# Kernel tuning notes

Hardware: AMD Instinct MI355X
Metric: run time of the kernel (lower is better)

## Reference

```python
import jax, jax.numpy as jnp
import numpy as np

B, N, C, H = 4, 1024, 768, 12
D = C // H
SCALE = D ** -0.5


def setup_inputs() -> dict:
    key = jax.random.key(0)
    k1, k2, k3, k4 = jax.random.split(key, 4)
    x1 = jax.random.normal(k1, (B, N, C), dtype=jnp.float32)
    x2 = jax.random.normal(k2, (B, N, C), dtype=jnp.float32)
    # shared (dual-stream) Linear2 weights, torch nn.Linear layout: [out, in]
    W_qkv = jax.random.normal(k3, (3 * C, C), dtype=jnp.float32) * (C ** -0.5)
    b_qkv = jnp.zeros((3 * C,), dtype=jnp.float32)
    W_proj = jax.random.normal(k4, (C, C), dtype=jnp.float32) * (C ** -0.5)
    b_proj = jnp.zeros((C,), dtype=jnp.float32)
    return {"x1": x1, "x2": x2, "W_qkv": W_qkv, "b_qkv": b_qkv,
            "W_proj": W_proj, "b_proj": b_proj}


def _split_qkv(x, W_qkv, b_qkv):
    qkv = (x @ W_qkv.T + b_qkv).reshape(B, N, 3, H, D)
    qkv = jnp.transpose(qkv, (2, 0, 3, 1, 4))  # [3,B,H,N,D]
    return qkv[0], qkv[1], qkv[2]


def reference(x1, x2, W_qkv, b_qkv, W_proj, b_proj):
    q1, k1, v1 = _split_qkv(x1, W_qkv, b_qkv)
    q2, k2, v2 = _split_qkv(x2, W_qkv, b_qkv)
    # two score maps, combined before a single shared softmax
    s1 = jnp.einsum("bhqd,bhkd->bhqk", q1 * SCALE, k1)
    s2 = jnp.einsum("bhqd,bhkd->bhqk", q2 * SCALE, k2)
    attn = jax.nn.softmax(s1 + s2, axis=-1)  # [B,H,N,N]
    # same attention matrix applied to both value streams
    o1 = jnp.einsum("bhqk,bhkd->bhqd", attn, v1)
    o2 = jnpum = jnp.einsum("bhqk,bhkd->bhqd", attn, v2) if False else jnp.einsum("bhqk,bhkd->bhqd", attn, v2)
    o1 = jnp.transpose(o1, (0, 2, 1, 3)).reshape(B, N, C)
    o2 = jnp.transpose(o2, (0, 2, 1, 3)).reshape(B, N, C)
    y1 = o1 @ W_proj.T + b_proj
    y2 = o2 @ W_proj.T + b_proj
    return y1, y2
```

## Files before the change

kernel.cpp:

```cpp
#include <hip/hip_runtime.h>
#include <hip/hip_bf16.h>


typedef __bf16 bf16x8 __attribute__((ext_vector_type(8)));
typedef __bf16 bf16x4 __attribute__((ext_vector_type(4)));
typedef float  f32x4  __attribute__((ext_vector_type(4)));

__device__ __forceinline__ bf16x8 cvt8(const float* p) {
    f32x4 f0 = *(const f32x4*)p;
    f32x4 f1 = *(const f32x4*)(p + 4);
    bf16x8 r;
    r[0] = (__bf16)f0[0]; r[1] = (__bf16)f0[1]; r[2] = (__bf16)f0[2]; r[3] = (__bf16)f0[3];
    r[4] = (__bf16)f1[0]; r[5] = (__bf16)f1[1]; r[6] = (__bf16)f1[2]; r[7] = (__bf16)f1[3];
    return r;
}

__device__ __forceinline__ void async16(const __bf16* g, __bf16* l) {
    __builtin_amdgcn_global_load_lds(
        (const __attribute__((address_space(1))) void*)g,
        (__attribute__((address_space(3))) void*)l, 16, 0, 0);
}

__global__ __launch_bounds__(256)
void cvt4_k(const float* __restrict__ x1, const float* __restrict__ x2,
            const float* __restrict__ wq, const float* __restrict__ wp,
            __bf16* __restrict__ xc, __bf16* __restrict__ wqc,
            __bf16* __restrict__ wpc)
{
    __shared__ __bf16 L[16][776];
    const int bid = blockIdx.x, t = threadIdx.x;
    const float* src; __bf16* dst; int G;
    if (bid < 256)      { src = x1; dst = xc;            G = bid; }
    else if (bid < 512) { src = x2; dst = xc + 3145728;  G = bid - 256; }
    else if (bid < 656) { src = wq; dst = wqc;           G = bid - 512; }
    else                { src = wp; dst = wpc;           G = bid - 656; }

    const float* sb = src + (size_t)G * 16 * 768;
#pragma unroll
    for (int k = 0; k < 6; k++) {
        int iv = k * 256 + t;
        int row = iv / 96, c8 = iv % 96;
        *(bf16x8*)&L[row][c8 * 8] = cvt8(sb + row * 768 + c8 * 8);
    }
    __syncthreads();
    __bf16* db = dst + (size_t)G * 12288;
#pragma unroll
    for (int k = 0; k < 6; k++) {
        int j = k * 256 + t;
        int r = j & 15, ks = (j >> 4) & 3, kt = j >> 6;
        *(bf16x8*)(db + (size_t)j * 8) = *(const bf16x8*)&L[r][kt * 32 + ks * 8];
    }
}

__global__ __launch_bounds__(256)
void cvt_kt(const float* __restrict__ src, __bf16* __restrict__ dst, int nrun) {
    int j = blockIdx.x * 256 + threadIdx.x;
    if (j >= nrun) return;
    const int r  = j & 15;
    const int ks = (j >> 4) & 3;
    const int t2 = j >> 6;
    const int kt = t2 % 24;
    const int G  = t2 / 24;
    *(bf16x8*)(dst + (size_t)j * 8) =
        cvt8(src + (size_t)(G * 16 + r) * 768 + kt * 32 + ks * 8);
}

__global__ __launch_bounds__(256)
void gemm_qkv_s(const __bf16* __restrict__ Xc, const __bf16* __restrict__ Wq,
                const float* __restrict__ bias,
                __bf16* __restrict__ qo, __bf16* __restrict__ ko,
                __bf16* __restrict__ vo)
{
    __shared__ __bf16 As[3][128 * 32];
    __shared__ __bf16 Bs[3][128 * 32];

    const int t = threadIdx.x, w = t >> 6, lane = t & 63;
    const int l15 = lane & 15, quad = lane >> 4;
    const int wm = w >> 1, wn = w & 1;

    const int bid  = blockIdx.x;
    const int xcd  = bid & 7;
    const int i6   = bid >> 3;
    const int pair = i6 / 18;
    const int gx   = i6 - pair * 18;
    const int p    = xcd * 8 + pair;
    const int gy   = p & 31;
    const int st   = p >> 5;

    const __bf16* Ab = Xc + (size_t)st * 3145728 + (size_t)(gy * 8) * 24 * 512;
    const __bf16* Bb = Wq + (size_t)(gx * 8) * 24 * 512;

    f32x4 acc[4][4];
#pragma unroll
    for (int mi = 0; mi < 4; mi++)
#pragma unroll
        for (int ni = 0; ni < 4; ni++) acc[mi][ni] = f32x4{0.f, 0.f, 0.f, 0.f};

    const int ga0 = w * 2, ga1 = w * 2 + 1;

#define QSTAGE(BUF, KT)                                                          \
    do {                                                                         \
        async16(Ab + ((size_t)ga0 * 24 + (KT)) * 512 + lane * 8,                 \
                &As[BUF][ga0 * 512 + lane * 8]);                                 \
        async16(Ab + ((size_t)ga1 * 24 + (KT)) * 512 + lane * 8,                 \
                &As[BUF][ga1 * 512 + lane * 8]);                                 \
        async16(Bb + ((size_t)ga0 * 24 + (KT)) * 512 + lane * 8,                 \
                &Bs[BUF][ga0 * 512 + lane * 8]);                                 \
        async16(Bb + ((size_t)ga1 * 24 + (KT)) * 512 + lane * 8,                 \
                &Bs[BUF][ga1 * 512 + lane * 8]);                                 \
    } while (0)

    QSTAGE(0, 0);

#pragma unroll 3
    for (int kt = 0; kt < 24; kt++) {
        const int cb = kt % 3;
        if (kt < 23) {
            QSTAGE((kt + 1) % 3, kt + 1);
            asm volatile("s_waitcnt vmcnt(4)" ::: "memory");
        } else {
            asm volatile("s_waitcnt vmcnt(0)" ::: "memory");
        }
        __builtin_amdgcn_s_barrier();
        __builtin_amdgcn_sched_barrier(0);

        bf16x8 af[4], bfr[4];
#pragma unroll
        for (int mi = 0; mi < 4; mi++)
            af[mi] = *(const bf16x8*)&As[cb][(wm * 4 + mi) * 512 + lane * 8];
#pragma unroll
        for (int ni = 0; ni < 4; ni++)
            bfr[ni] = *(const bf16x8*)&Bs[cb][(wn * 4 + ni) * 512 + lane * 8];
#pragma unroll
        for (int mi = 0; mi < 4; mi++)
#pragma unroll
            for (int ni = 0; ni < 4; ni++)
                acc[mi][ni] = __builtin_amdgcn_mfma_f32_16x16x32_bf16(af[mi], bfr[ni], acc[mi][ni], 0, 0, 0);
    }
#undef QSTAGE

    const int which = (gx * 128) / 768;

    if (which == 2) {
#pragma unroll
        for (int ni = 0; ni < 4; ni++) {
            int j = gx * 128 + wn * 64 + ni * 16 + l15;
            int c = j - 1536;
            int h = c >> 6, d = c & 63;
            float bj = bias[j];
#pragma unroll
            for (int mi = 0; mi < 4; mi++) {
                int row0 = gy * 128 + wm * 64 + mi * 16 + quad * 4;
                int b = row0 >> 10, tok0 = row0 & 1023;
                bf16x4 pv;
#pragma unroll
                for (int r = 0; r < 4; r++) pv[r] = (__bf16)(acc[mi][ni][r] + bj);
                *(bf16x4*)&vo[((size_t)((st * 4 + b) * 12 + h) * 64 + d) * 1024 + tok0] = pv;
            }
        }
    } else {
#pragma unroll
        for (int ni = 0; ni < 4; ni++) {
            int j     = gx * 128 + wn * 64 + ni * 16 + l15;
            int c     = j - which * 768;
            int h = c >> 6, d = c & 63;
            float bj  = bias[j];
#pragma unroll
            for (int mi = 0; mi < 4; mi++) {
#pragma unroll
                for (int r = 0; r < 4; r++) {
                    int row = gy * 128 + wm * 64 + mi * 16 + quad * 4 + r;
                    int b = row >> 10, tok = row & 1023;
                    float val = acc[mi][ni][r] + bj;
                    if (which == 0)
                        qo[((size_t)((st * 4 + b) * 12 + h) * 1024 + tok) * 64 + d] = (__bf16)(val * 0.125f);
                    else
                        ko[((size_t)((st * 4 + b) * 12 + h) * 1024 + tok) * 64 + d] = (__bf16)val;
                }
            }
        }
    }
}

__global__ __launch_bounds__(256)
void gemm_proj(const __bf16* __restrict__ A, const __bf16* __restrict__ Wp,
               const float* __restrict__ bias, float* __restrict__ out)
{
    __shared__ __bf16 As[3][64 * 32];
    __shared__ __bf16 Bs[3][128 * 32];

    const int t = threadIdx.x, w = t >> 6, lane = t & 63;
    const int l15 = lane & 15, quad = lane >> 4;
    const int wm = w >> 1, wn = w & 1;
    const int gx = blockIdx.x, gy = blockIdx.y;

    const __bf16* Ab = A  + (size_t)(gy * 4) * 24 * 512;
    const __bf16* Bb = Wp + (size_t)(gx * 8) * 24 * 512;

    f32x4 acc[2][4];
#pragma unroll
    for (int mi = 0; mi < 2; mi++)
#pragma unroll
        for (int ni = 0; ni < 4; ni++) acc[mi][ni] = f32x4{0.f, 0.f, 0.f, 0.f};

#define PSTAGE(BUF, KT)                                                          \
    do {                                                                         \
        async16(Ab + ((size_t)w * 24 + (KT)) * 512 + lane * 8,                   \
                &As[BUF][w * 512 + lane * 8]);                                   \
        async16(Bb + ((size_t)(w * 2) * 24 + (KT)) * 512 + lane * 8,             \
                &Bs[BUF][(w * 2) * 512 + lane * 8]);                             \
        async16(Bb + ((size_t)(w * 2 + 1) * 24 + (KT)) * 512 + lane * 8,         \
                &Bs[BUF][(w * 2 + 1) * 512 + lane * 8]);                         \
    } while (0)

    PSTAGE(0, 0);

#pragma unroll 3
    for (int kt = 0; kt < 24; kt++) {
        const int cb = kt % 3;
        if (kt < 23) {
            PSTAGE((kt + 1) % 3, kt + 1);
            asm volatile("s_waitcnt vmcnt(3)" ::: "memory");
        } else {
            asm volatile("s_waitcnt vmcnt(0)" ::: "memory");
        }
        __builtin_amdgcn_s_barrier();
        __builtin_amdgcn_sched_barrier(0);

        bf16x8 af[2], bfr[4];
#pragma unroll
        for (int mi = 0; mi < 2; mi++)
            af[mi] = *(const bf16x8*)&As[cb][(wm * 2 + mi) * 512 + lane * 8];
#pragma unroll
        for (int ni = 0; ni < 4; ni++)
            bfr[ni] = *(const bf16x8*)&Bs[cb][(wn * 4 + ni) * 512 + lane * 8];
#pragma unroll
        for (int mi = 0; mi < 2; mi++)
#pragma unroll
            for (int ni = 0; ni < 4; ni++)
                acc[mi][ni] = __builtin_amdgcn_mfma_f32_16x16x32_bf16(af[mi], bfr[ni], acc[mi][ni], 0, 0, 0);
    }
#undef PSTAGE

#pragma unroll
    for (int ni = 0; ni < 4; ni++) {
        int col  = gx * 128 + wn * 64 + ni * 16 + l15;
        float bj = bias[col];
#pragma unroll
        for (int mi = 0; mi < 2; mi++)
#pragma unroll
            for (int r = 0; r < 4; r++) {
                int row = gy * 64 + (wm * 2 + mi) * 16 + quad * 4 + r;
                out[(size_t)row * 768 + col] = acc[mi][ni][r] + bj;
            }
    }
}

__global__ __launch_bounds__(128, 2)
void attn_k(const __bf16* __restrict__ qws, const __bf16* __restrict__ kws,
            const __bf16* __restrict__ vws, __bf16* __restrict__ ows)
{
    __shared__ __bf16 Ks[2][2][2][2][512];
    __shared__ __bf16 Vs[2][2][4][512];
    __shared__ __bf16 Ps[2][2][16 * 72];

    const int g  = blockIdx.x;
    const int qt = g / 48;
    const int bh = g % 48;
    const int b = bh / 12, h = bh % 12;
    const int t = threadIdx.x, w = t >> 6, lane = t & 63;
    const int l15 = lane & 15, quad = lane >> 4;

    const size_t head_off = (size_t)bh * 65536;
    const size_t ss       = (size_t)48 * 65536;

    bf16x8 qf[2][2][2];
#pragma unroll
    for (int set = 0; set < 2; set++)
#pragma unroll
        for (int s = 0; s < 2; s++)
#pragma unroll
            for (int kk = 0; kk < 2; kk++)
                qf[set][s][kk] = *(const bf16x8*)(qws + s * ss + head_off
                    + (size_t)(qt * 64 + w * 32 + set * 16 + l15) * 64 + kk * 32 + quad * 8);

    float lsum[2] = {0.f, 0.f};
    f32x4 accO[2][2][4];
#pragma unroll
    for (int set = 0; set < 2; set++)
#pragma unroll
        for (int s = 0; s < 2; s++)
#pragma unroll
            for (int mi = 0; mi < 4; mi++) accO[set][s][mi] = f32x4{0.f, 0.f, 0.f, 0.f};

    const __bf16* kbase = kws + head_off;
    const __bf16* vbase = vws + head_off;

#define STAGE_TILE(BUF, KEYB)                                                   \
    do {                                                                        \
        if (w == 0) {                                                           \
            _Pragma("unroll")                                                   \
            for (int i = 0; i < 8; i++) {                                       \
                const int s = i >> 2, kk = (i >> 1) & 1, mi = i & 1;            \
                async16(kbase + s * ss + (size_t)((KEYB) + mi * 16 + l15) * 64  \
                            + kk * 32 + quad * 8,                               \
                        &Ks[BUF][s][kk][mi][lane * 8]);                         \
            }                                                                   \
        } else {                                                                \
            _Pragma("unroll")                                                   \
            for (int i = 0; i < 8; i++) {                                       \
                const int s = i >> 2, mi = i & 3;                               \
                async16(vbase + s * ss + (size_t)(mi * 16 + l15) * 1024         \
                            + (KEYB) + quad * 8,                                \
                        &Vs[BUF][s][mi][lane * 8]);                             \
            }                                                                   \
        }                                                                       \
    } while (0)

    STAGE_TILE(0, 0);
    __syncthreads();

#pragma unroll 2
    for (int kt = 0; kt < 32; kt++) {
        const int cb = kt & 1, nb = cb ^ 1;

        if (kt < 31) STAGE_TILE(nb, (kt + 1) * 32);

        f32x4 accS[2][2];
#pragma unroll
        for (int set = 0; set < 2; set++)
#pragma unroll
            for (int mi = 0; mi < 2; mi++) accS[set][mi] = f32x4{0.f, 0.f, 0.f, 0.f};
        __builtin_amdgcn_s_setprio(1);
#pragma unroll
        for (int s = 0; s < 2; s++)
#pragma unroll
            for (int kk = 0; kk < 2; kk++) {
                bf16x8 kf0 = *(const bf16x8*)&Ks[cb][s][kk][0][lane * 8];
                bf16x8 kf1 = *(const bf16x8*)&Ks[cb][s][kk][1][lane * 8];
#pragma unroll
                for (int set = 0; set < 2; set++) {
                    accS[set][0] = __builtin_amdgcn_mfma_f32_16x16x32_bf16(kf0, qf[set][s][kk], accS[set][0], 0, 0, 0);
                    accS[set][1] = __builtin_amdgcn_mfma_f32_16x16x32_bf16(kf1, qf[set][s][kk], accS[set][1], 0, 0, 0);
                }
            }
        __builtin_amdgcn_s_setprio(0);

#pragma unroll
        for (int set = 0; set < 2; set++) {
            float rs = 0.f;
#pragma unroll
            for (int mi = 0; mi < 2; mi++) {
                bf16x4 pk;
#pragma unroll
                for (int r = 0; r < 4; r++) {
                    float pv = __expf(accS[set][mi][r]);
                    pk[r] = (__bf16)pv;
                    rs += pv;
                }
                *(bf16x4*)&Ps[w][set][l15 * 72 + mi * 16 + quad * 4] = pk;
            }
            lsum[set] += rs;
        }

        bf16x8 pa0 = *(const bf16x8*)&Ps[w][0][l15 * 72 + quad * 8];
        bf16x8 pa1 = *(const bf16x8*)&Ps[w][1][l15 * 72 + quad * 8];
        __builtin_amdgcn_s_setprio(1);
#pragma unroll
        for (int s = 0; s < 2; s++)
#pragma unroll
            for (int mi = 0; mi < 4; mi++) {
                bf16x8 vf = *(const bf16x8*)&Vs[cb][s][mi][lane * 8];
                accO[0][s][mi] = __builtin_amdgcn_mfma_f32_16x16x32_bf16(vf, pa0, accO[0][s][mi], 0, 0, 0);
                accO[1][s][mi] = __builtin_amdgcn_mfma_f32_16x16x32_bf16(vf, pa1, accO[1][s][mi], 0, 0, 0);
            }
        __builtin_amdgcn_s_setprio(0);

        __syncthreads();
    }
#undef STAGE_TILE

#pragma unroll
    for (int set = 0; set < 2; set++) {
        float l = lsum[set];
        l += __shfl_xor(l, 16);
        l += __shfl_xor(l, 32);
        float il = 1.f / l;

        const int tok = qt * 64 + w * 32 + set * 16 + l15;
#pragma unroll
        for (int s = 0; s < 2; s++)
#pragma unroll
            for (int mi = 0; mi < 4; mi++) {
                bf16x4 ov;
#pragma unroll
                for (int r = 0; r < 4; r++) ov[r] = (__bf16)(accO[set][s][mi][r] * il);
                const int row = (s * 4 + b) * 1024 + tok;
                const int c   = h * 64 + mi * 16 + quad * 4;
                const size_t off = ((size_t)(row >> 4) * 24 + (c >> 5)) * 512
                                 + ((c >> 3) & 3) * 128 + (row & 15) * 8 + (c & 7);
                *(bf16x4*)&ows[off] = ov;
            }
    }
}

extern "C" void kernel_launch(void* const* d_in, const int* in_sizes, int n_in,
                              void* d_out, int out_size, void* d_ws, size_t ws_size,
                              hipStream_t stream)
{
    const float* x1    = (const float*)d_in[0];
    const float* x2    = (const float*)d_in[1];
    const float* Wqkv  = (const float*)d_in[2];
    const float* bqkv  = (const float*)d_in[3];
    const float* Wproj = (const float*)d_in[4];
    const float* bproj = (const float*)d_in[5];
    float* out = (float*)d_out;

    const size_t qkv_elems = (size_t)2 * 4 * 12 * 1024 * 64;
    __bf16* q_ws = (__bf16*)d_ws;
    __bf16* k_ws = q_ws + qkv_elems;
    __bf16* v_ws = k_ws + qkv_elems;
    __bf16* pool = v_ws + qkv_elems;
    __bf16* o_ws = pool;
    __bf16* Wqc  = pool + 3145728;
    __bf16* Xc   = (__bf16*)d_out;

    const bool big = ws_size >= (size_t)(4 * qkv_elems + 589824) * sizeof(__bf16);
    __bf16* Wpc = big ? (pool + qkv_elems)
                      : q_ws;

    cvt4_k<<<big ? 704 : 656, 256, 0, stream>>>(x1, x2, Wqkv, Wproj, Xc, Wqc, Wpc);
    gemm_qkv_s<<<1152, 256, 0, stream>>>(Xc, Wqc, bqkv, q_ws, k_ws, v_ws);
    attn_k<<<768, 128, 0, stream>>>(q_ws, k_ws, v_ws, o_ws);
    if (!big) cvt_kt<<<288, 256, 0, stream>>>(Wproj, Wpc, 73728);
    gemm_proj<<<dim3(6, 128), 256, 0, stream>>>(o_ws, Wpc, bproj, out);
}
```

Before: 206.9 us.

## Split attention key range across two wave pairs with LDS reduction

The attention kernel now launches 256 threads per block. Two pairs of waves each handle half of the key sequence (512 keys) for the same 64 queries, and their partial outputs and row sums are merged through shared memory at the end. The double-buffered async prefetch is replaced by a single-buffered load followed by a vmcnt wait and barrier each iteration. This doubles the waves available to hide latency per query tile, at the cost of exposed load latency with no prefetch, an extra LDS reduction, and a larger shared-memory footprint that may limit occupancy.

```diff
diff --git a/kernel.cpp b/kernel.cpp
--- a/kernel.cpp
+++ b/kernel.cpp
@@ -256,13 +256,15 @@
     }
 }
 
-__global__ __launch_bounds__(128, 2)
+__global__ __launch_bounds__(256, 3)
 void attn_k(const __bf16* __restrict__ qws, const __bf16* __restrict__ kws,
             const __bf16* __restrict__ vws, __bf16* __restrict__ ows)
 {
-    __shared__ __bf16 Ks[2][2][2][2][512];
-    __shared__ __bf16 Vs[2][2][4][512];
-    __shared__ __bf16 Ps[2][2][16 * 72];
+    __shared__ __align__(16) char SMEM[51200];
+    __bf16* KF  = (__bf16*)SMEM;
+    __bf16* VF  = (__bf16*)(SMEM + 16384);
+    __bf16* PS  = (__bf16*)(SMEM + 32768);
+    float*  RED = (float*)SMEM;
 
     const int g  = blockIdx.x;
     const int qt = g / 48;
@@ -270,6 +272,7 @@
     const int b = bh / 12, h = bh % 12;
     const int t = threadIdx.x, w = t >> 6, lane = t & 63;
     const int l15 = lane & 15, quad = lane >> 4;
+    const int p = w >> 1, qsub = w & 1;
 
     const size_t head_off = (size_t)bh * 65536;
     const size_t ss       = (size_t)48 * 65536;
@@ -282,7 +285,7 @@
 #pragma unroll
             for (int kk = 0; kk < 2; kk++)
                 qf[set][s][kk] = *(const bf16x8*)(qws + s * ss + head_off
-                    + (size_t)(qt * 64 + w * 32 + set * 16 + l15) * 64 + kk * 32 + quad * 8);
+                    + (size_t)(qt * 64 + qsub * 32 + set * 16 + l15) * 64 + kk * 32 + quad * 8);
 
     float lsum[2] = {0.f, 0.f};
     f32x4 accO[2][2][4];
@@ -296,35 +299,29 @@
     const __bf16* kbase = kws + head_off;
     const __bf16* vbase = vws + head_off;
 
-#define STAGE_TILE(BUF, KEYB)                                                   \
-    do {                                                                        \
-        if (w == 0) {                                                           \
-            _Pragma("unroll")                                                   \
-            for (int i = 0; i < 8; i++) {                                       \
-                const int s = i >> 2, kk = (i >> 1) & 1, mi = i & 1;            \
-                async16(kbase + s * ss + (size_t)((KEYB) + mi * 16 + l15) * 64  \
-                            + kk * 32 + quad * 8,                               \
-                        &Ks[BUF][s][kk][mi][lane * 8]);                         \
-            }                                                                   \
-        } else {                                                                \
-            _Pragma("unroll")                                                   \
-            for (int i = 0; i < 8; i++) {                                       \
-                const int s = i >> 2, mi = i & 3;                               \
-                async16(vbase + s * ss + (size_t)(mi * 16 + l15) * 1024         \
-                            + (KEYB) + quad * 8,                                \
-                        &Vs[BUF][s][mi][lane * 8]);                             \
-            }                                                                   \
-        }                                                                       \
-    } while (0)
-
-    STAGE_TILE(0, 0);
-    __syncthreads();
-
-#pragma unroll 2
-    for (int kt = 0; kt < 32; kt++) {
-        const int cb = kt & 1, nb = cb ^ 1;
-
-        if (kt < 31) STAGE_TILE(nb, (kt + 1) * 32);
+    for (int kt = 0; kt < 16; kt++) {
+        const int keyb = p * 512 + kt * 32;
+
+        if (qsub == 0) {
+#pragma unroll
+            for (int i = 0; i < 8; i++) {
+                const int s = i >> 2, kk = (i >> 1) & 1, mi = i & 1;
+                async16(kbase + s * ss + (size_t)(keyb + mi * 16 + l15) * 64
+                            + kk * 32 + quad * 8,
+                        KF + (size_t)(p * 8 + s * 4 + kk * 2 + mi) * 512 + lane * 8);
+            }
+        } else {
+#pragma unroll
+            for (int i = 0; i < 8; i++) {
+                const int s = i >> 2, mi = i & 3;
+                async16(vbase + s * ss + (size_t)(mi * 16 + l15) * 1024
+                            + keyb + quad * 8,
+                        VF + (size_t)(p * 8 + s * 4 + mi) * 512 + lane * 8);
+            }
+        }
+        asm volatile("s_waitcnt vmcnt(0)" ::: "memory");
+        __builtin_amdgcn_s_barrier();
+        __builtin_amdgcn_sched_barrier(0);
 
         f32x4 accS[2][2];
 #pragma unroll
@@ -336,8 +333,8 @@
         for (int s = 0; s < 2; s++)
 #pragma unroll
             for (int kk = 0; kk < 2; kk++) {
-                bf16x8 kf0 = *(const bf16x8*)&Ks[cb][s][kk][0][lane * 8];
-                bf16x8 kf1 = *(const bf16x8*)&Ks[cb][s][kk][1][lane * 8];
+                bf16x8 kf0 = *(const bf16x8*)&KF[(size_t)(p * 8 + s * 4 + kk * 2 + 0) * 512 + lane * 8];
+                bf16x8 kf1 = *(const bf16x8*)&KF[(size_t)(p * 8 + s * 4 + kk * 2 + 1) * 512 + lane * 8];
 #pragma unroll
                 for (int set = 0; set < 2; set++) {
                     accS[set][0] = __builtin_amdgcn_mfma_f32_16x16x32_bf16(kf0, qf[set][s][kk], accS[set][0], 0, 0, 0);
@@ -358,27 +355,59 @@
                     pk[r] = (__bf16)pv;
                     rs += pv;
                 }
-                *(bf16x4*)&Ps[w][set][l15 * 72 + mi * 16 + quad * 4] = pk;
+                *(bf16x4*)&PS[(size_t)(w * 2 + set) * 1152 + l15 * 72 + mi * 16 + quad * 4] = pk;
             }
             lsum[set] += rs;
         }
 
-        bf16x8 pa0 = *(const bf16x8*)&Ps[w][0][l15 * 72 + quad * 8];
-        bf16x8 pa1 = *(const bf16x8*)&Ps[w][1][l15 * 72 + quad * 8];
+        bf16x8 pa0 = *(const bf16x8*)&PS[(size_t)(w * 2 + 0) * 1152 + l15 * 72 + quad * 8];
+        bf16x8 pa1 = *(const bf16x8*)&PS[(size_t)(w * 2 + 1) * 1152 + l15 * 72 + quad * 8];
         __builtin_amdgcn_s_setprio(1);
 #pragma unroll
         for (int s = 0; s < 2; s++)
 #pragma unroll
             for (int mi = 0; mi < 4; mi++) {
-                bf16x8 vf = *(const bf16x8*)&Vs[cb][s][mi][lane * 8];
+                bf16x8 vf = *(const bf16x8*)&VF[(size_t)(p * 8 + s * 4 + mi) * 512 + lane * 8];
                 accO[0][s][mi] = __builtin_amdgcn_mfma_f32_16x16x32_bf16(vf, pa0, accO[0][s][mi], 0, 0, 0);
                 accO[1][s][mi] = __builtin_amdgcn_mfma_f32_16x16x32_bf16(vf, pa1, accO[1][s][mi], 0, 0, 0);
             }
         __builtin_amdgcn_s_setprio(0);
 
-        __syncthreads();
-    }
-#undef STAGE_TILE
+        __builtin_amdgcn_s_barrier();
+    }
+
+    __syncthreads();
+    if (p == 1) {
+        float* R = RED + (size_t)(qsub * 64 + lane) * 66;
+        int idx = 0;
+#pragma unroll
+        for (int set = 0; set < 2; set++)
+#pragma unroll
+            for (int s = 0; s < 2; s++)
+#pragma unroll
+                for (int mi = 0; mi < 4; mi++)
+#pragma unroll
+                    for (int r = 0; r < 4; r++) R[idx++] = accO[set][s][mi][r];
+        R[64] = lsum[0];
+        R[65] = lsum[1];
+    }
+    __syncthreads();
+    if (p == 1) return;
+
+    {
+        const float* R = RED + (size_t)(qsub * 64 + lane) * 66;
+        int idx = 0;
+#pragma unroll
+        for (int set = 0; set < 2; set++)
+#pragma unroll
+            for (int s = 0; s < 2; s++)
+#pragma unroll
+                for (int mi = 0; mi < 4; mi++)
+#pragma unroll
+                    for (int r = 0; r < 4; r++) accO[set][s][mi][r] += R[idx++];
+        lsum[0] += R[64];
+        lsum[1] += R[65];
+    }
 
 #pragma unroll
     for (int set = 0; set < 2; set++) {
@@ -387,7 +416,7 @@
         l += __shfl_xor(l, 32);
         float il = 1.f / l;
 
-        const int tok = qt * 64 + w * 32 + set * 16 + l15;
+        const int tok = qt * 64 + qsub * 32 + set * 16 + l15;
 #pragma unroll
         for (int s = 0; s < 2; s++)
 #pragma unroll
@@ -431,7 +460,7 @@
 
     cvt4_k<<<big ? 704 : 656, 256, 0, stream>>>(x1, x2, Wqkv, Wproj, Xc, Wqc, Wpc);
     gemm_qkv_s<<<1152, 256, 0, stream>>>(Xc, Wqc, bqkv, q_ws, k_ws, v_ws);
-    attn_k<<<768, 128, 0, stream>>>(q_ws, k_ws, v_ws, o_ws);
+    attn_k<<<768, 256, 0, stream>>>(q_ws, k_ws, v_ws, o_ws);
     if (!big) cvt_kt<<<288, 256, 0, stream>>>(Wproj, Wpc, 73728);
     gemm_proj<<<dim3(6, 128), 256, 0, stream>>>(o_ws, Wpc, bproj, out);
 }
```

Result: slower. 214.4 us (+3.6%).

## Split attention into single-wave blocks with single-buffered K/V and waitcnt pipelining

Applied to the files above, without the earlier changes.

The attention kernel moves from 128-thread blocks (two waves sharing double-buffered K/V tiles and a block barrier) to 64-thread single-wave blocks covering 32 queries each, launched as twice as many blocks. Each wave now loads its own K and V tiles into single buffers. It orders them with explicit vmcnt/lgkmcnt waits instead of __syncthreads, issuing the next K load after the QK MFMAs and the next V load after the PV MFMAs. This removes block-level barriers and raises block count and occupancy, but doubles global/L2 traffic for K/V because two waves no longer share tiles. The hand-counted waitcnt values are fragile.

```diff
diff --git a/kernel.cpp b/kernel.cpp
--- a/kernel.cpp
+++ b/kernel.cpp
@@ -256,24 +256,51 @@
     }
 }
 
-__global__ __launch_bounds__(128, 2)
+__global__ __launch_bounds__(64)
 void attn_k(const __bf16* __restrict__ qws, const __bf16* __restrict__ kws,
             const __bf16* __restrict__ vws, __bf16* __restrict__ ows)
 {
-    __shared__ __bf16 Ks[2][2][2][2][512];
-    __shared__ __bf16 Vs[2][2][4][512];
-    __shared__ __bf16 Ps[2][2][16 * 72];
+    __shared__ __bf16 KF[2][2][2][512];
+    __shared__ __bf16 VF[2][4][512];
+    __shared__ __bf16 PS[2][16 * 72];
 
     const int g  = blockIdx.x;
     const int qt = g / 48;
     const int bh = g % 48;
     const int b = bh / 12, h = bh % 12;
-    const int t = threadIdx.x, w = t >> 6, lane = t & 63;
+    const int lane = threadIdx.x;
     const int l15 = lane & 15, quad = lane >> 4;
 
     const size_t head_off = (size_t)bh * 65536;
     const size_t ss       = (size_t)48 * 65536;
 
+    const __bf16* kbase = kws + head_off;
+    const __bf16* vbase = vws + head_off;
+
+#define STAGE_K(KEYB)                                                           \
+    do {                                                                        \
+        _Pragma("unroll")                                                       \
+        for (int i = 0; i < 8; i++) {                                           \
+            const int s = i >> 2, kk = (i >> 1) & 1, mi = i & 1;                \
+            async16(kbase + s * ss + (size_t)((KEYB) + mi * 16 + l15) * 64      \
+                        + kk * 32 + quad * 8,                                   \
+                    &KF[s][kk][mi][lane * 8]);                                  \
+        }                                                                       \
+    } while (0)
+#define STAGE_V(KEYB)                                                           \
+    do {                                                                        \
+        _Pragma("unroll")                                                       \
+        for (int i = 0; i < 8; i++) {                                           \
+            const int s = i >> 2, mi = i & 3;                                   \
+            async16(vbase + s * ss + (size_t)(mi * 16 + l15) * 1024             \
+                        + (KEYB) + quad * 8,                                    \
+                    &VF[s][mi][lane * 8]);                                      \
+        }                                                                       \
+    } while (0)
+
+    STAGE_K(0);
+    STAGE_V(0);
+
     bf16x8 qf[2][2][2];
 #pragma unroll
     for (int set = 0; set < 2; set++)
@@ -282,7 +309,7 @@
 #pragma unroll
             for (int kk = 0; kk < 2; kk++)
                 qf[set][s][kk] = *(const bf16x8*)(qws + s * ss + head_off
-                    + (size_t)(qt * 64 + w * 32 + set * 16 + l15) * 64 + kk * 32 + quad * 8);
+                    + (size_t)(qt * 32 + set * 16 + l15) * 64 + kk * 32 + quad * 8);
 
     float lsum[2] = {0.f, 0.f};
     f32x4 accO[2][2][4];
@@ -293,38 +320,14 @@
 #pragma unroll
             for (int mi = 0; mi < 4; mi++) accO[set][s][mi] = f32x4{0.f, 0.f, 0.f, 0.f};
 
-    const __bf16* kbase = kws + head_off;
-    const __bf16* vbase = vws + head_off;
-
-#define STAGE_TILE(BUF, KEYB)                                                   \
-    do {                                                                        \
-        if (w == 0) {                                                           \
-            _Pragma("unroll")                                                   \
-            for (int i = 0; i < 8; i++) {                                       \
-                const int s = i >> 2, kk = (i >> 1) & 1, mi = i & 1;            \
-                async16(kbase + s * ss + (size_t)((KEYB) + mi * 16 + l15) * 64  \
-                            + kk * 32 + quad * 8,                               \
-                        &Ks[BUF][s][kk][mi][lane * 8]);                         \
-            }                                                                   \
-        } else {                                                                \
-            _Pragma("unroll")                                                   \
-            for (int i = 0; i < 8; i++) {                                       \
-                const int s = i >> 2, mi = i & 3;                               \
-                async16(vbase + s * ss + (size_t)(mi * 16 + l15) * 1024         \
-                            + (KEYB) + quad * 8,                                \
-                        &Vs[BUF][s][mi][lane * 8]);                             \
-            }                                                                   \
-        }                                                                       \
-    } while (0)
-
-    STAGE_TILE(0, 0);
-    __syncthreads();
-
-#pragma unroll 2
+    asm volatile("s_waitcnt vmcnt(0)" ::: "memory");
+    __builtin_amdgcn_sched_barrier(0);
+
     for (int kt = 0; kt < 32; kt++) {
-        const int cb = kt & 1, nb = cb ^ 1;
-
-        if (kt < 31) STAGE_TILE(nb, (kt + 1) * 32);
+        if (kt > 0) {
+            asm volatile("s_waitcnt vmcnt(8)" ::: "memory");
+            __builtin_amdgcn_sched_barrier(0);
+        }
 
         f32x4 accS[2][2];
 #pragma unroll
@@ -336,8 +339,8 @@
         for (int s = 0; s < 2; s++)
 #pragma unroll
             for (int kk = 0; kk < 2; kk++) {
-                bf16x8 kf0 = *(const bf16x8*)&Ks[cb][s][kk][0][lane * 8];
-                bf16x8 kf1 = *(const bf16x8*)&Ks[cb][s][kk][1][lane * 8];
+                bf16x8 kf0 = *(const bf16x8*)&KF[s][kk][0][lane * 8];
+                bf16x8 kf1 = *(const bf16x8*)&KF[s][kk][1][lane * 8];
 #pragma unroll
                 for (int set = 0; set < 2; set++) {
                     accS[set][0] = __builtin_amdgcn_mfma_f32_16x16x32_bf16(kf0, qf[set][s][kk], accS[set][0], 0, 0, 0);
@@ -345,6 +348,12 @@
                 }
             }
         __builtin_amdgcn_s_setprio(0);
+
+        if (kt < 31) {
+            asm volatile("s_waitcnt lgkmcnt(0)" ::: "memory");
+            __builtin_amdgcn_sched_barrier(0);
+            STAGE_K((kt + 1) * 32);
+        }
 
 #pragma unroll
         for (int set = 0; set < 2; set++) {
@@ -358,27 +367,39 @@
                     pk[r] = (__bf16)pv;
                     rs += pv;
                 }
-                *(bf16x4*)&Ps[w][set][l15 * 72 + mi * 16 + quad * 4] = pk;
+                *(bf16x4*)&PS[set][l15 * 72 + mi * 16 + quad * 4] = pk;
             }
             lsum[set] += rs;
         }
 
-        bf16x8 pa0 = *(const bf16x8*)&Ps[w][0][l15 * 72 + quad * 8];
-        bf16x8 pa1 = *(const bf16x8*)&Ps[w][1][l15 * 72 + quad * 8];
+        if (kt < 31) {
+            asm volatile("s_waitcnt vmcnt(8)" ::: "memory");
+        } else {
+            asm volatile("s_waitcnt vmcnt(0)" ::: "memory");
+        }
+        __builtin_amdgcn_sched_barrier(0);
+
+        bf16x8 pa0 = *(const bf16x8*)&PS[0][l15 * 72 + quad * 8];
+        bf16x8 pa1 = *(const bf16x8*)&PS[1][l15 * 72 + quad * 8];
         __builtin_amdgcn_s_setprio(1);
 #pragma unroll
         for (int s = 0; s < 2; s++)
 #pragma unroll
             for (int mi = 0; mi < 4; mi++) {
-                bf16x8 vf = *(const bf16x8*)&Vs[cb][s][mi][lane * 8];
+                bf16x8 vf = *(const bf16x8*)&VF[s][mi][lane * 8];
                 accO[0][s][mi] = __builtin_amdgcn_mfma_f32_16x16x32_bf16(vf, pa0, accO[0][s][mi], 0, 0, 0);
                 accO[1][s][mi] = __builtin_amdgcn_mfma_f32_16x16x32_bf16(vf, pa1, accO[1][s][mi], 0, 0, 0);
             }
         __builtin_amdgcn_s_setprio(0);
 
-        __syncthreads();
-    }
-#undef STAGE_TILE
+        if (kt < 31) {
+            asm volatile("s_waitcnt lgkmcnt(0)" ::: "memory");
+            __builtin_amdgcn_sched_barrier(0);
+            STAGE_V((kt + 1) * 32);
+        }
+    }
+#undef STAGE_K
+#undef STAGE_V
 
 #pragma unroll
     for (int set = 0; set < 2; set++) {
@@ -387,7 +408,7 @@
         l += __shfl_xor(l, 32);
         float il = 1.f / l;
 
-        const int tok = qt * 64 + w * 32 + set * 16 + l15;
+        const int tok = qt * 32 + set * 16 + l15;
 #pragma unroll
         for (int s = 0; s < 2; s++)
 #pragma unroll
@@ -431,7 +452,7 @@
 
     cvt4_k<<<big ? 704 : 656, 256, 0, stream>>>(x1, x2, Wqkv, Wproj, Xc, Wqc, Wpc);
     gemm_qkv_s<<<1152, 256, 0, stream>>>(Xc, Wqc, bqkv, q_ws, k_ws, v_ws);
-    attn_k<<<768, 128, 0, stream>>>(q_ws, k_ws, v_ws, o_ws);
+    attn_k<<<1536, 64, 0, stream>>>(q_ws, k_ws, v_ws, o_ws);
     if (!big) cvt_kt<<<288, 256, 0, stream>>>(Wproj, Wpc, 73728);
     gemm_proj<<<dim3(6, 128), 256, 0, stream>>>(o_ws, Wpc, bproj, out);
 }
```

Result: slower. 247.0 us (+19.4%).
